# Kernel tuning notes

Measured on AMD Instinct MI355X. Metric: run time of the kernel, lower is better.

The kernel has to match this reference:

```python
import jax, jax.numpy as jnp
import numpy as np

ALPHA = 0.8   # dice-score exponent
BETA = 0.2    # class-prob exponent
EPS = 1e-4    # dice denominator epsilon (SparseInst dice_score)


def _hungarian_max(cost):
    """Rectangular linear_sum_assignment(maximize=True) for a numpy (n,m) cost.
    Pads to square, runs the O(s^3) Hungarian algorithm with potentials.
    Returns (rows, cols) of length min(n,m), rows sorted (matches scipy)."""
    n, m = cost.shape
    s = max(n, m)
    c = np.zeros((s, s), dtype=np.float64)
    c[:n, :m] = -cost  # maximize -> minimize
    INF = 1e18
    u = np.zeros(s + 1)
    v = np.zeros(s + 1)
    p = np.zeros(s + 1, dtype=np.int64)
    way = np.zeros(s + 1, dtype=np.int64)
    for i in range(1, s + 1):
        p[0] = i
        j0 = 0
        minv = np.full(s + 1, INF)
        used = np.zeros(s + 1, dtype=bool)
        while True:
            used[j0] = True
            i0 = p[j0]
            cur = c[i0 - 1, :] - u[i0] - v[1:]
            free = ~used[1:]
            upd = free & (cur < minv[1:])
            minv[1:][upd] = cur[upd]
            way[1:][upd] = j0
            cand = np.where(free, minv[1:], INF)
            j1 = int(np.argmin(cand)) + 1
            delta = cand[j1 - 1]
            u[p[used]] += delta
            v[used] -= delta
            minv[~used] -= delta
            j0 = j1
            if p[j0] == 0:
                break
        while j0:
            j1 = way[j0]
            p[j0] = p[j1]
            j0 = j1
    rows, cols = [], []
    for j in range(1, s + 1):
        i = p[j]
        if i - 1 < n and j - 1 < m:
            rows.append(i - 1)
            cols.append(j - 1)
    order = np.argsort(np.asarray(rows))
    return np.asarray(rows)[order], np.asarray(cols)[order]


def _cost_matrix(pred_masks, pred_logits, tgt_masks, tgt_ids):
    B, N, H, W = pred_masks.shape
    T = tgt_masks.shape[0]
    pm = jax.nn.sigmoid(pred_masks.astype(jnp.float32)).reshape(B * N, H * W)
    # bilinear resize (align_corners=False / half-pixel) of GT masks to pred grid
    tm = jax.image.resize(tgt_masks.astype(jnp.float32), (T, H, W), method='linear')
    tm = tm.reshape(T, H * W)
    # dice score: 2<p,t> / (|p|^2 + |t|^2 + eps)   -> (B*N, T)
    num = 2.0 * jnp.einsum('qd,td->qt', pm, tm)
    den = jnp.sum(pm * pm, axis=-1)[:, None] + jnp.sum(tm * tm, axis=-1)[None, :]
    dice = num / (den + EPS)
    prob = jax.nn.sigmoid(pred_logits.astype(jnp.float32)).reshape(B * N, -1)[:, tgt_ids]
    C = dice ** ALPHA * prob ** BETA
    return C.reshape(B, N, T)


_cost_matrix_jit = jax.jit(_cost_matrix)


def setup_inputs() -> dict:
    key = jax.random.key(0)
    k1, k2, k3, k4 = jax.random.split(key, 4)
    B, N, H, W = 16, 100, 128, 128
    T, NC = 320, 80
    return {
        'pred_masks': jax.random.normal(k1, (B, N, H, W), dtype=jnp.float32),
        'pred_logits': jax.random.normal(k2, (B, N, NC), dtype=jnp.float32),
        'tgt_masks': jax.random.uniform(k3, (T, 2 * H, 2 * W), dtype=jnp.float32),
        'tgt_ids': jax.random.randint(k4, (T,), 0, NC, dtype=jnp.int64) if jax.config.jax_enable_x64 else jax.random.randint(k4, (T,), 0, NC, dtype=jnp.int32),
    }


def reference(pred_masks, pred_logits, tgt_masks, tgt_ids):
    B, N = pred_masks.shape[:2]
    T = tgt_masks.shape[0]
    per_img = T // B  # uniform sizes per image (stands in for [len(v['masks'])])
    C = _cost_matrix_jit(pred_masks, pred_logits, tgt_masks, tgt_ids)
    Cn = np.asarray(jax.device_get(C))
    rows, cols = [], []
    for b in range(B):
        r, c = _hungarian_max(Cn[b, :, b * per_img:(b + 1) * per_img])
        rows.append(r)
        cols.append(c)
    rows = jnp.asarray(np.stack(rows), dtype=jnp.int32)  # (B, per_img)
    cols = jnp.asarray(np.stack(cols), dtype=jnp.int32)  # (B, per_img)
    return C, rows, cols
```

## Files before the change

kernel.cpp:

```cpp
#include <hip/hip_runtime.h>
#include <math.h>

#define NB 16
#define NP 100
#define NT 320
#define NCLS 80
#define WO 128
#define HW 16384
#define QT 1600
#define PI 20
#define KSPLIT 8
#define KSLICE 2048
#define BK 64
#define KTILES 32
#define SRC_W 256
#define BM 64
#define BN 160
#define CH 16

typedef _Float16 half8v __attribute__((ext_vector_type(8)));
typedef float f32x4 __attribute__((ext_vector_type(4)));

#define GLOAD_LDS16(gp, lp) __builtin_amdgcn_global_load_lds(                         \
    (const __attribute__((address_space(1))) void*)(gp),                              \
    (__attribute__((address_space(3))) void*)(lp), 16, 0, 0)

__device__ __forceinline__ float sigf(float x){ return 1.0f/(1.0f+expf(-x)); }
__device__ __forceinline__ float sigfast(float x){ return 1.0f/(1.0f+__expf(-x)); }

__device__ __forceinline__ void mkw128(int i, float* w, int* ix){
  int j0 = 2*i - 1;
  ix[0]=j0; ix[1]=j0+1; ix[2]=j0+2; ix[3]=j0+3;
  w[0]=0.125f; w[1]=0.375f; w[2]=0.375f; w[3]=0.125f;
  if (i == 0){ ix[0]=0; w[0]=0.0f; w[1]=3.0f/7.0f; w[2]=3.0f/7.0f; w[3]=1.0f/7.0f; }
  if (i == 127){ ix[3]=255; w[3]=0.0f; w[0]=1.0f/7.0f; w[1]=3.0f/7.0f; w[2]=3.0f/7.0f; }
}

__global__ __launch_bounds__(256) void k_downsample(const float* __restrict__ tgt,
                                                    _Float16* __restrict__ tm,
                                                    float* __restrict__ tqpart){
  const int blk = blockIdx.x;
  const int t = blk >> 3;
  const int c = blk & 7;
  const int x = threadIdx.x;
  const int oy0 = c * CH;
  const int r0 = 2*oy0 - 1;
  const float* src = tgt + (size_t)t * (SRC_W*SRC_W);
  __shared__ float vbuf[CH][SRC_W];
  __shared__ float wred[4];

  float cc[34];
  #pragma unroll
  for (int li = 0; li < 34; ++li){
    int r = r0 + li; r = r < 0 ? 0 : (r > 255 ? 255 : r);
    cc[li] = src[r*SRC_W + x];
  }
  #pragma unroll
  for (int dy = 0; dy < CH; ++dy){
    int oy = oy0 + dy;
    float w0=0.125f, w1=0.375f, w2=0.375f, w3=0.125f;
    if (oy == 0){ w0=0.0f; w1=3.0f/7.0f; w2=3.0f/7.0f; w3=1.0f/7.0f; }
    if (oy == 127){ w3=0.0f; w0=1.0f/7.0f; w1=3.0f/7.0f; w2=3.0f/7.0f; }
    vbuf[dy][x] = w0*cc[2*dy] + w1*cc[2*dy+1] + w2*cc[2*dy+2] + w3*cc[2*dy+3];
  }
  __syncthreads();

  float ssq = 0.f;
  _Float16* dst = tm + (size_t)t * HW + (size_t)oy0 * WO;
  #pragma unroll
  for (int i = 0; i < 8; ++i){
    int e = x + 256*i;
    int oy = e >> 7;
    int ox = e & 127;
    float w[4]; int ix[4];
    mkw128(ox, w, ix);
    float val = w[0]*vbuf[oy][ix[0]] + w[1]*vbuf[oy][ix[1]]
              + w[2]*vbuf[oy][ix[2]] + w[3]*vbuf[oy][ix[3]];
    dst[oy*WO + ox] = (_Float16)val;
    ssq += val*val;
  }
  for (int off=32; off; off>>=1) ssq += __shfl_xor(ssq, off);
  if ((x & 63) == 0) wred[x >> 6] = ssq;
  __syncthreads();
  if (x == 0) tqpart[c*NT + t] = wred[0]+wred[1]+wred[2]+wred[3];
}

__global__ __launch_bounds__(512, 4) void k_gemm(const float* __restrict__ A,
                                                 const _Float16* __restrict__ Bm,
                                                 float* __restrict__ part,
                                                 float* __restrict__ pqpart){
  __shared__ _Float16 As[2][BM*BK];
  __shared__ _Float16 Bs[2][BN*BK];
  const int tid = threadIdx.x;
  const int lane = tid & 63;
  const int wid = tid >> 6;
  const int rg = wid >> 1;
  const int cg = wid & 1;
  const int q0 = blockIdx.x * BM;
  const int t0 = blockIdx.y * BN;
  const int z  = blockIdx.z;
  const int ks = z * KSLICE;

  const int ar = tid >> 3;
  const int ac8 = tid & 7;
  const float* ap = A + (size_t)(q0 + ar) * HW + ks + ac8*8;
  const int awoff = ar*BK + ((ac8 ^ (ar & 7)) * 8);

  f32x4 acc[5];
  #pragma unroll
  for (int n = 0; n < 5; ++n) acc[n] = (f32x4){0.f,0.f,0.f,0.f};
  float pqs = 0.f;

  #pragma unroll
  for (int i = 0; i < 3; ++i){
    int g = i*512 + tid;
    if (g < 1280){
      int row = g >> 3, s = g & 7;
      GLOAD_LDS16(Bm + (size_t)(t0 + row)*HW + ks + ((s ^ (row & 7)) * 8),
                  &Bs[0][(size_t)g*8]);
    }
  }
  {
    float4 v0 = *(const float4*)(ap);
    float4 v1 = *(const float4*)(ap + 4);
    float s0 = sigfast(v0.x), s1 = sigfast(v0.y), s2 = sigfast(v0.z), s3 = sigfast(v0.w);
    float s4 = sigfast(v1.x), s5 = sigfast(v1.y), s6 = sigfast(v1.z), s7 = sigfast(v1.w);
    pqs += s0*s0 + s1*s1 + s2*s2 + s3*s3 + s4*s4 + s5*s5 + s6*s6 + s7*s7;
    half8v hh = { (_Float16)s0, (_Float16)s1, (_Float16)s2, (_Float16)s3,
                  (_Float16)s4, (_Float16)s5, (_Float16)s6, (_Float16)s7 };
    *(half8v*)&As[0][awoff] = hh;
  }
  float4 aCur0 = *(const float4*)(ap + BK);
  float4 aCur1 = *(const float4*)(ap + BK + 4);
  asm volatile("s_waitcnt vmcnt(2) lgkmcnt(0)" ::: "memory");
  __builtin_amdgcn_s_barrier();

  for (int kt = 0; kt < KTILES; ++kt){
    const int cur = kt & 1, nxt = cur ^ 1;
    if (kt + 1 < KTILES){
      #pragma unroll
      for (int i = 0; i < 3; ++i){
        int g = i*512 + tid;
        if (g < 1280){
          int row = g >> 3, s = g & 7;
          GLOAD_LDS16(Bm + (size_t)(t0 + row)*HW + ks + (kt+1)*BK + ((s ^ (row & 7)) * 8),
                      &Bs[nxt][(size_t)g*8]);
        }
      }
    }
    float4 aNext0, aNext1;
    if (kt + 2 < KTILES){
      const float* apn = ap + (kt+2)*BK;
      aNext0 = *(const float4*)(apn);
      aNext1 = *(const float4*)(apn + 4);
    }
    #pragma unroll
    for (int s = 0; s < 2; ++s){
      half8v af, bf[5];
      {
        int r = rg*16 + (lane & 15);
        int c = s*4 + (lane >> 4);
        af = *(const half8v*)&As[cur][r*BK + ((c ^ (r & 7)) * 8)];
      }
      #pragma unroll
      for (int n = 0; n < 5; ++n){
        int r = cg*80 + n*16 + (lane & 15);
        int c = s*4 + (lane >> 4);
        bf[n] = *(const half8v*)&Bs[cur][r*BK + ((c ^ (r & 7)) * 8)];
      }
      #pragma unroll
      for (int n = 0; n < 5; ++n)
        acc[n] = __builtin_amdgcn_mfma_f32_16x16x32_f16(af, bf[n], acc[n], 0, 0, 0);
    }
    if (kt + 1 < KTILES){
      float s0 = sigfast(aCur0.x), s1 = sigfast(aCur0.y), s2 = sigfast(aCur0.z), s3 = sigfast(aCur0.w);
      float s4 = sigfast(aCur1.x), s5 = sigfast(aCur1.y), s6 = sigfast(aCur1.z), s7 = sigfast(aCur1.w);
      pqs += s0*s0 + s1*s1 + s2*s2 + s3*s3 + s4*s4 + s5*s5 + s6*s6 + s7*s7;
      half8v hh = { (_Float16)s0, (_Float16)s1, (_Float16)s2, (_Float16)s3,
                    (_Float16)s4, (_Float16)s5, (_Float16)s6, (_Float16)s7 };
      *(half8v*)&As[nxt][awoff] = hh;
      aCur0 = aNext0; aCur1 = aNext1;
    }
    if (kt + 2 < KTILES){
      asm volatile("s_waitcnt vmcnt(2) lgkmcnt(0)" ::: "memory");
    } else {
      asm volatile("s_waitcnt vmcnt(0) lgkmcnt(0)" ::: "memory");
    }
    __builtin_amdgcn_s_barrier();
  }

  float* op = part + (size_t)z * (QT*NT);
  {
    int qb = q0 + rg*16 + (lane >> 4)*4;
    #pragma unroll
    for (int n = 0; n < 5; ++n){
      int t = t0 + cg*80 + n*16 + (lane & 15);
      #pragma unroll
      for (int r = 0; r < 4; ++r)
        op[(size_t)(qb + r)*NT + t] = acc[n][r];
    }
  }
  if (blockIdx.y == 0){
    pqs += __shfl_xor(pqs, 1);
    pqs += __shfl_xor(pqs, 2);
    pqs += __shfl_xor(pqs, 4);
    if ((tid & 7) == 0) pqpart[z*QT + q0 + ar] = pqs;
  }
}

__global__ __launch_bounds__(256) void k_cost(const float* __restrict__ part,
                                              const float* __restrict__ pqpart,
                                              const float* __restrict__ tqpart,
                                              const float* __restrict__ logits,
                                              const int* __restrict__ ids,
                                              float* __restrict__ Cout){
  int idx = blockIdx.x * 256 + threadIdx.x;
  int q = idx / NT;
  int t = idx - q * NT;
  float num = 0.f;
  #pragma unroll
  for (int s = 0; s < KSPLIT; ++s) num += part[(size_t)s * (QT*NT) + idx];
  num *= 2.0f;
  float pqv = 0.f;
  #pragma unroll
  for (int s = 0; s < KSPLIT; ++s) pqv += pqpart[s * QT + q];
  float tqv = 0.f;
  #pragma unroll
  for (int s = 0; s < 8; ++s) tqv += tqpart[s * NT + t];
  float den = pqv + tqv + 1e-4f;
  float dice = num / den;
  float prob = sigf(logits[q * NCLS + ids[t]]);
  Cout[idx] = powf(dice, 0.8f) * powf(prob, 0.2f);
}

__global__ __launch_bounds__(64) void k_hung(const float* __restrict__ C,
                                             float* __restrict__ rows_out,
                                             float* __restrict__ cols_out){
  const int b = blockIdx.x;
  const int lane = threadIdx.x;
  __shared__ float negC[PI*NP];
  __shared__ double u[PI+1];
  __shared__ int p[NP+1];
  __shared__ int way[NP+1];
  for (int e = lane; e < PI*NP; e += 64){
    int i = e / NP, j = e - i*NP;
    negC[e] = -C[(size_t)(b*NP + j)*NT + (b*PI + i)];
  }
  if (lane <= PI) u[lane] = 0.0;
  for (int j = lane; j <= NP; j += 64){ p[j] = 0; way[j] = 0; }
  __syncthreads();
  const int jA = lane + 1;
  const int jB = lane + 65;
  const bool hasB = (jB <= NP);
  double vA = 0.0, vB = 0.0;
  const double INFD = 1e18;
  for (int i = 1; i <= PI; ++i){
    if (lane == 0) p[0] = i;
    __syncthreads();
    double mvA = INFD, mvB = INFD;
    bool usA = false, usB = false;
    int j0 = 0;
    int jbrk = 0;
    while (true){
      if (jA == j0) usA = true;
      if (hasB && jB == j0) usB = true;
      int i0 = p[j0];
      double ui0 = u[i0];
      double candA = INFD, candB = INFD;
      if (!usA){
        double cur = (double)negC[(i0-1)*NP + (jA-1)] - ui0 - vA;
        if (cur < mvA){ mvA = cur; way[jA] = j0; }
        candA = mvA;
      }
      if (hasB && !usB){
        double cur = (double)negC[(i0-1)*NP + (jB-1)] - ui0 - vB;
        if (cur < mvB){ mvB = cur; way[jB] = j0; }
        candB = mvB;
      }
      double bv; int bj;
      if (candB < candA){ bv = candB; bj = jB; } else { bv = candA; bj = jA; }
      for (int off = 32; off; off >>= 1){
        double ov = __shfl_xor(bv, off);
        int oj = __shfl_xor(bj, off);
        if (ov < bv || (ov == bv && oj < bj)){ bv = ov; bj = oj; }
      }
      const double delta = bv;
      if (usA){ int pj = p[jA]; u[pj] += delta; vA -= delta; }
      else mvA -= delta;
      if (hasB){
        if (usB){ int pj = p[jB]; u[pj] += delta; vB -= delta; }
        else mvB -= delta;
      }
      if (lane == 0) u[p[0]] += delta;
      __syncthreads();
      j0 = bj;
      if (p[j0] == 0){ jbrk = j0; break; }
    }
    __syncthreads();
    if (lane == 0){
      int j0a = jbrk;
      while (j0a){
        int jp = way[j0a];
        p[j0a] = p[jp];
        j0a = jp;
      }
    }
    __syncthreads();
  }
  if (lane == 0){
    int cnt = 0;
    for (int j = 1; j <= NP; ++j){
      int pi = p[j];
      if (pi != 0){
        rows_out[b*PI + cnt] = (float)(j - 1);
        cols_out[b*PI + cnt] = (float)(pi - 1);
        ++cnt;
      }
    }
  }
}

extern "C" void kernel_launch(void* const* d_in, const int* in_sizes, int n_in,
                              void* d_out, int out_size, void* d_ws, size_t ws_size,
                              hipStream_t stream){
  const float* pred_masks  = (const float*)d_in[0];
  const float* pred_logits = (const float*)d_in[1];
  const float* tgt_masks   = (const float*)d_in[2];
  const int*   tgt_ids     = (const int*)d_in[3];
  float* out = (float*)d_out;
  char* ws = (char*)d_ws;
  _Float16* Th  = (_Float16*)ws;
  float* tqpart = (float*)(ws + (size_t)NT*HW*2);
  float* pqpart = (float*)(ws + (size_t)NT*HW*2 + 16384);
  float* part   = (float*)(ws + (size_t)NT*HW*2 + 16384 + 65536);

  k_downsample<<<NT*8, 256, 0, stream>>>(tgt_masks, Th, tqpart);
  dim3 g(QT/BM, NT/BN, KSPLIT);
  k_gemm<<<g, 512, 0, stream>>>(pred_masks, Th, part, pqpart);
  k_cost<<<(QT*NT)/256, 256, 0, stream>>>(part, pqpart, tqpart, pred_logits, tgt_ids, out);
  k_hung<<<NB, 64, 0, stream>>>(out, out + (size_t)QT*NT, out + (size_t)QT*NT + NT);
}
```

Measured before the change: 125.8 us.

## Precompute sigmoid fp16 prediction masks in separate kernel, DMA both GEMM operands to LDS

Adds a pre-pass kernel that applies sigmoid to the prediction masks, writes them as fp16 and computes per-query squared norms. The GEMM then loads A tiles with direct global-to-LDS loads, the same way as B, instead of repeating the fp32 load and sigmoid in every N-tile block (twice, since grid.y is 2). The intent is to halve A read traffic inside the GEMM and drop per-block sigmoid ALU work. The cost is an extra kernel launch plus an extra 52MB fp32 read and 52MB fp16 write/reread pass.

```diff
diff --git a/kernel.cpp b/kernel.cpp
--- a/kernel.cpp
+++ b/kernel.cpp
@@ -18,6 +18,7 @@
 #define BN 160
 #define CH 16
 
+typedef _Float16 half4v __attribute__((ext_vector_type(4)));
 typedef _Float16 half8v __attribute__((ext_vector_type(8)));
 typedef float f32x4 __attribute__((ext_vector_type(4)));
 
@@ -34,6 +35,29 @@
   w[0]=0.125f; w[1]=0.375f; w[2]=0.375f; w[3]=0.125f;
   if (i == 0){ ix[0]=0; w[0]=0.0f; w[1]=3.0f/7.0f; w[2]=3.0f/7.0f; w[3]=1.0f/7.0f; }
   if (i == 127){ ix[3]=255; w[3]=0.0f; w[0]=1.0f/7.0f; w[1]=3.0f/7.0f; w[2]=3.0f/7.0f; }
+}
+
+__global__ __launch_bounds__(256) void k_sig(const float* __restrict__ A,
+                                             _Float16* __restrict__ Ah,
+                                             float* __restrict__ pq){
+  const int q = blockIdx.x;
+  const int tid = threadIdx.x;
+  const float4* src = (const float4*)(A + (size_t)q * HW);
+  half4v* dst = (half4v*)(Ah + (size_t)q * HW);
+  float ss = 0.f;
+  #pragma unroll
+  for (int i = 0; i < 16; ++i){
+    float4 v = src[i*256 + tid];
+    float s0 = sigfast(v.x), s1 = sigfast(v.y), s2 = sigfast(v.z), s3 = sigfast(v.w);
+    ss += s0*s0 + s1*s1 + s2*s2 + s3*s3;
+    half4v hh = { (_Float16)s0, (_Float16)s1, (_Float16)s2, (_Float16)s3 };
+    dst[i*256 + tid] = hh;
+  }
+  __shared__ float wred[4];
+  for (int off = 32; off; off >>= 1) ss += __shfl_xor(ss, off);
+  if ((tid & 63) == 0) wred[tid >> 6] = ss;
+  __syncthreads();
+  if (tid == 0) pq[q] = wred[0] + wred[1] + wred[2] + wred[3];
 }
 
 __global__ __launch_bounds__(256) void k_downsample(const float* __restrict__ tgt,
@@ -85,10 +109,9 @@
   if (x == 0) tqpart[c*NT + t] = wred[0]+wred[1]+wred[2]+wred[3];
 }
 
-__global__ __launch_bounds__(512, 4) void k_gemm(const float* __restrict__ A,
+__global__ __launch_bounds__(512, 4) void k_gemm(const _Float16* __restrict__ Ah,
                                                  const _Float16* __restrict__ Bm,
-                                                 float* __restrict__ part,
-                                                 float* __restrict__ pqpart){
+                                                 float* __restrict__ part){
   __shared__ _Float16 As[2][BM*BK];
   __shared__ _Float16 Bs[2][BN*BK];
   const int tid = threadIdx.x;
@@ -101,16 +124,14 @@
   const int z  = blockIdx.z;
   const int ks = z * KSLICE;
 
-  const int ar = tid >> 3;
-  const int ac8 = tid & 7;
-  const float* ap = A + (size_t)(q0 + ar) * HW + ks + ac8*8;
-  const int awoff = ar*BK + ((ac8 ^ (ar & 7)) * 8);
+  const int arow = tid >> 3, aslot = tid & 7;
+  const _Float16* agp = Ah + (size_t)(q0 + arow)*HW + ks + ((aslot ^ (arow & 7)) * 8);
 
   f32x4 acc[5];
   #pragma unroll
   for (int n = 0; n < 5; ++n) acc[n] = (f32x4){0.f,0.f,0.f,0.f};
-  float pqs = 0.f;
-
+
+  GLOAD_LDS16(agp, &As[0][(size_t)tid*8]);
   #pragma unroll
   for (int i = 0; i < 3; ++i){
     int g = i*512 + tid;
@@ -120,24 +141,13 @@
                   &Bs[0][(size_t)g*8]);
     }
   }
-  {
-    float4 v0 = *(const float4*)(ap);
-    float4 v1 = *(const float4*)(ap + 4);
-    float s0 = sigfast(v0.x), s1 = sigfast(v0.y), s2 = sigfast(v0.z), s3 = sigfast(v0.w);
-    float s4 = sigfast(v1.x), s5 = sigfast(v1.y), s6 = sigfast(v1.z), s7 = sigfast(v1.w);
-    pqs += s0*s0 + s1*s1 + s2*s2 + s3*s3 + s4*s4 + s5*s5 + s6*s6 + s7*s7;
-    half8v hh = { (_Float16)s0, (_Float16)s1, (_Float16)s2, (_Float16)s3,
-                  (_Float16)s4, (_Float16)s5, (_Float16)s6, (_Float16)s7 };
-    *(half8v*)&As[0][awoff] = hh;
-  }
-  float4 aCur0 = *(const float4*)(ap + BK);
-  float4 aCur1 = *(const float4*)(ap + BK + 4);
-  asm volatile("s_waitcnt vmcnt(2) lgkmcnt(0)" ::: "memory");
+  asm volatile("s_waitcnt vmcnt(0)" ::: "memory");
   __builtin_amdgcn_s_barrier();
 
   for (int kt = 0; kt < KTILES; ++kt){
     const int cur = kt & 1, nxt = cur ^ 1;
     if (kt + 1 < KTILES){
+      GLOAD_LDS16(agp + (kt+1)*BK, &As[nxt][(size_t)tid*8]);
       #pragma unroll
       for (int i = 0; i < 3; ++i){
         int g = i*512 + tid;
@@ -148,12 +158,6 @@
         }
       }
     }
-    float4 aNext0, aNext1;
-    if (kt + 2 < KTILES){
-      const float* apn = ap + (kt+2)*BK;
-      aNext0 = *(const float4*)(apn);
-      aNext1 = *(const float4*)(apn + 4);
-    }
     #pragma unroll
     for (int s = 0; s < 2; ++s){
       half8v af, bf[5];
@@ -172,20 +176,7 @@
       for (int n = 0; n < 5; ++n)
         acc[n] = __builtin_amdgcn_mfma_f32_16x16x32_f16(af, bf[n], acc[n], 0, 0, 0);
     }
-    if (kt + 1 < KTILES){
-      float s0 = sigfast(aCur0.x), s1 = sigfast(aCur0.y), s2 = sigfast(aCur0.z), s3 = sigfast(aCur0.w);
-      float s4 = sigfast(aCur1.x), s5 = sigfast(aCur1.y), s6 = sigfast(aCur1.z), s7 = sigfast(aCur1.w);
-      pqs += s0*s0 + s1*s1 + s2*s2 + s3*s3 + s4*s4 + s5*s5 + s6*s6 + s7*s7;
-      half8v hh = { (_Float16)s0, (_Float16)s1, (_Float16)s2, (_Float16)s3,
-                    (_Float16)s4, (_Float16)s5, (_Float16)s6, (_Float16)s7 };
-      *(half8v*)&As[nxt][awoff] = hh;
-      aCur0 = aNext0; aCur1 = aNext1;
-    }
-    if (kt + 2 < KTILES){
-      asm volatile("s_waitcnt vmcnt(2) lgkmcnt(0)" ::: "memory");
-    } else {
-      asm volatile("s_waitcnt vmcnt(0) lgkmcnt(0)" ::: "memory");
-    }
+    asm volatile("s_waitcnt vmcnt(0)" ::: "memory");
     __builtin_amdgcn_s_barrier();
   }
 
@@ -200,16 +191,10 @@
         op[(size_t)(qb + r)*NT + t] = acc[n][r];
     }
   }
-  if (blockIdx.y == 0){
-    pqs += __shfl_xor(pqs, 1);
-    pqs += __shfl_xor(pqs, 2);
-    pqs += __shfl_xor(pqs, 4);
-    if ((tid & 7) == 0) pqpart[z*QT + q0 + ar] = pqs;
-  }
 }
 
 __global__ __launch_bounds__(256) void k_cost(const float* __restrict__ part,
-                                              const float* __restrict__ pqpart,
+                                              const float* __restrict__ pq,
                                               const float* __restrict__ tqpart,
                                               const float* __restrict__ logits,
                                               const int* __restrict__ ids,
@@ -221,13 +206,10 @@
   #pragma unroll
   for (int s = 0; s < KSPLIT; ++s) num += part[(size_t)s * (QT*NT) + idx];
   num *= 2.0f;
-  float pqv = 0.f;
-  #pragma unroll
-  for (int s = 0; s < KSPLIT; ++s) pqv += pqpart[s * QT + q];
   float tqv = 0.f;
   #pragma unroll
   for (int s = 0; s < 8; ++s) tqv += tqpart[s * NT + t];
-  float den = pqv + tqv + 1e-4f;
+  float den = pq[q] + tqv + 1e-4f;
   float dice = num / den;
   float prob = sigf(logits[q * NCLS + ids[t]]);
   Cout[idx] = powf(dice, 0.8f) * powf(prob, 0.2f);
@@ -330,13 +312,16 @@
   float* out = (float*)d_out;
   char* ws = (char*)d_ws;
   _Float16* Th  = (_Float16*)ws;
-  float* tqpart = (float*)(ws + (size_t)NT*HW*2);
-  float* pqpart = (float*)(ws + (size_t)NT*HW*2 + 16384);
-  float* part   = (float*)(ws + (size_t)NT*HW*2 + 16384 + 65536);
-
+  size_t off = (size_t)NT*HW*2;
+  float* tqpart = (float*)(ws + off);            off += 16384;
+  float* pq     = (float*)(ws + off);            off += 16384;
+  _Float16* Ah  = (_Float16*)(ws + off);         off += (size_t)QT*HW*2;
+  float* part   = (float*)(ws + off);
+
+  k_sig<<<QT, 256, 0, stream>>>(pred_masks, Ah, pq);
   k_downsample<<<NT*8, 256, 0, stream>>>(tgt_masks, Th, tqpart);
   dim3 g(QT/BM, NT/BN, KSPLIT);
-  k_gemm<<<g, 512, 0, stream>>>(pred_masks, Th, part, pqpart);
-  k_cost<<<(QT*NT)/256, 256, 0, stream>>>(part, pqpart, tqpart, pred_logits, tgt_ids, out);
+  k_gemm<<<g, 512, 0, stream>>>(Ah, Th, part);
+  k_cost<<<(QT*NT)/256, 256, 0, stream>>>(part, pq, tqpart, pred_logits, tgt_ids, out);
   k_hung<<<NB, 64, 0, stream>>>(out, out + (size_t)QT*NT, out + (size_t)QT*NT + NT);
 }
```

Measured after the change: 127.1 us. No clear change (+1.1%).
